# Optimization experiments

Hardware: AMD Instinct MI355X
Metric: run time of the kernel (lower is better)

## Reference

```python
import jax, jax.numpy as jnp
import numpy as np

GRID_H, GRID_W = 496, 432  # config.grid_shape
BN_EPS = 1e-5


def setup_inputs() -> dict:
    key = jax.random.key(0)
    k1, k2, k3 = jax.random.split(key, 3)
    B, D, P, N, C = 4, 4, 12000, 100, 64
    x = jax.random.normal(k1, (B, D, P, N), dtype=jnp.float32)
    indices = jax.random.randint(k2, (B, P, 2), 0, GRID_W, dtype=jnp.int32)
    W = jax.random.normal(k3, (C, D), dtype=jnp.float32) / np.sqrt(D)
    gamma = jnp.ones((C,), dtype=jnp.float32)
    beta = jnp.zeros((C,), dtype=jnp.float32)
    return {"x": x, "indices": indices, "W": W, "gamma": gamma, "beta": beta}


def reference(x, indices, W, gamma, beta):
    # 1x1 conv (bias=False): [B, D, P, N] x [C, D] -> [B, C, P, N]
    y = jnp.einsum('bdpn,cd->bcpn', x, W)
    # BatchNorm2d (training-mode batch statistics, biased variance)
    mean = jnp.mean(y, axis=(0, 2, 3), keepdims=True)
    var = jnp.var(y, axis=(0, 2, 3), keepdims=True)
    y = (y - mean) * jax.lax.rsqrt(var + BN_EPS)
    y = y * gamma.reshape(1, -1, 1, 1) + beta.reshape(1, -1, 1, 1)
    y = jax.nn.relu(y)
    # MaxPool2d((1, N)) then squeeze -> [B, C, P]
    p = jnp.max(y, axis=3)
    # scatter: per-batch index_add into flattened BEV grid
    pillars = jnp.transpose(p, (0, 2, 1))  # [B, P, C]
    flat_idx = indices[..., 0] * GRID_W + indices[..., 1]  # [B, P]
    grid = jax.vmap(
        lambda v, i: jax.ops.segment_sum(v, i, num_segments=GRID_H * GRID_W)
    )(pillars, flat_idx)  # [B, H*W, C]
    C = pillars.shape[-1]
    out = grid.reshape(-1, GRID_H, GRID_W, C)
    return jnp.transpose(out, (0, 3, 1, 2))  # [B, C, H, W]
```

## Files before the change

### kernel.cpp

```cpp
#include <hip/hip_runtime.h>

#define B_ 4
#define D_ 4
#define P_ 12000
#define N_ 100
#define C_ 64
#define GH 496
#define GW 432
#define PN (P_*N_)
#define HW (GH*GW)
#define WPB 12
#define PPB (WPB*8)
#define GRID_F (B_*(P_/PPB))
#define OVFCAP 4096

static constexpr size_t OFF_ST    = 0;
static constexpr size_t OFF_PART  = 512;
static constexpr size_t PART_BYTES= 14*(size_t)GRID_F*4;
static constexpr size_t OFF_SLOT  = (OFF_PART + PART_BYTES + 255) & ~(size_t)255;
static constexpr size_t SLOT_BYTES= (size_t)B_*HW*4;
static constexpr size_t OFF_OVFC  = OFF_SLOT + SLOT_BYTES;
static constexpr size_t OFF_OVF   = OFF_OVFC + 64;
static constexpr size_t OVF_BYTES = (size_t)OVFCAP*4;
static constexpr size_t OFF_U     = (OFF_OVF + OVF_BYTES + 255) & ~(size_t)255;
static constexpr size_t U_BYTES   = (size_t)B_*P_*C_*4;

template<int CTRL>
__device__ __forceinline__ float dppmax(float v) {
    int s = __builtin_amdgcn_update_dpp(0, __float_as_int(v), CTRL, 0xf, 0xf, true);
    return fmaxf(v, __int_as_float(s));
}

__global__ __launch_bounds__(256) void k_init(int4* __restrict__ slot4,
                                              int* __restrict__ ovfcnt) {
    int i = blockIdx.x*256 + threadIdx.x;
    int4 neg1; neg1.x = neg1.y = neg1.z = neg1.w = -1;
    slot4[i] = neg1;
    if (i == 0) *ovfcnt = 0;
}

__global__ __launch_bounds__(256) void k_alloc(const int* __restrict__ idx,
                                               int* __restrict__ slot,
                                               int* __restrict__ ovf,
                                               int* __restrict__ ovfcnt) {
    const int BPB = (P_ + 255)/256;
    int b = blockIdx.x / BPB;
    int p = (blockIdx.x % BPB)*256 + threadIdx.x;
    if (p >= P_) return;
    size_t bp = (size_t)b*P_ + p;
    int h = idx[bp*2], w = idx[bp*2 + 1];
    int cell = h*GW + w;
    int old = atomicMax(&slot[(size_t)b*HW + cell], p);
    if (old != -1) {
        int loser = (old < p) ? old : p;
        int at = atomicAdd(ovfcnt, 1);
        if (at < OVFCAP) ovf[at] = b*P_ + loser;
    }
}

__global__ __launch_bounds__(768) void k_fused(const float* __restrict__ x,
                                               const float* __restrict__ Wm,
                                               float* __restrict__ partials,
                                               float* __restrict__ uraw) {
    __shared__ float tr[WPB][8*65 + 8];
    __shared__ float red[WPB][14];
    const int BPB = P_/PPB;
    int b    = blockIdx.x / BPB;
    int pblk = (blockIdx.x % BPB)*PPB;
    int lane = threadIdx.x & 63;
    int wv   = threadIdx.x >> 6;
    int pl   = lane >> 3;
    int oct  = lane & 7;
    int p    = pblk + wv*8 + pl;
    const float* xb = x + (size_t)b*D_*PN + (size_t)p*N_;

    float4 xq[3][4];
    #pragma unroll
    for (int j = 0; j < 3; ++j) {
        int n = 4*oct + 32*j;
        #pragma unroll
        for (int d = 0; d < 4; ++d)
            xq[j][d] = *reinterpret_cast<const float4*>(xb + n + (size_t)d*PN);
    }
    float x13[4];
    #pragma unroll
    for (int d = 0; d < 4; ++d)
        x13[d] = (oct < 4) ? xb[96 + oct + (size_t)d*PN] : xq[0][d].x;

    {
        float s0=0,s1=0,s2=0,s3=0;
        float m00=0,m01=0,m02=0,m03=0,m11=0,m12=0,m13=0,m22=0,m23=0,m33=0;
        #pragma unroll
        for (int j = 0; j < 3; ++j) {
            #pragma unroll
            for (int e = 0; e < 4; ++e) {
                float x0 = ((const float*)&xq[j][0])[e];
                float x1 = ((const float*)&xq[j][1])[e];
                float x2 = ((const float*)&xq[j][2])[e];
                float x3 = ((const float*)&xq[j][3])[e];
                s0+=x0; s1+=x1; s2+=x2; s3+=x3;
                m00=fmaf(x0,x0,m00); m01=fmaf(x0,x1,m01); m02=fmaf(x0,x2,m02); m03=fmaf(x0,x3,m03);
                m11=fmaf(x1,x1,m11); m12=fmaf(x1,x2,m12); m13=fmaf(x1,x3,m13);
                m22=fmaf(x2,x2,m22); m23=fmaf(x2,x3,m23); m33=fmaf(x3,x3,m33);
            }
        }
        if (oct < 4) {
            float x0=x13[0], x1=x13[1], x2=x13[2], x3=x13[3];
            s0+=x0; s1+=x1; s2+=x2; s3+=x3;
            m00=fmaf(x0,x0,m00); m01=fmaf(x0,x1,m01); m02=fmaf(x0,x2,m02); m03=fmaf(x0,x3,m03);
            m11=fmaf(x1,x1,m11); m12=fmaf(x1,x2,m12); m13=fmaf(x1,x3,m13);
            m22=fmaf(x2,x2,m22); m23=fmaf(x2,x3,m23); m33=fmaf(x3,x3,m33);
        }
        float v[14] = {s0,s1,s2,s3,m00,m01,m02,m03,m11,m12,m13,m22,m23,m33};
        #pragma unroll
        for (int j = 0; j < 14; ++j) {
            float t = v[j];
            #pragma unroll
            for (int off = 32; off; off >>= 1) t += __shfl_down(t, off);
            if (lane == 0) red[wv][j] = t;
        }
        __syncthreads();
        if (threadIdx.x < 14) {
            int j = threadIdx.x;
            float t = 0.f;
            #pragma unroll
            for (int w2 = 0; w2 < WPB; ++w2) t += red[w2][j];
            partials[(size_t)j*GRID_F + blockIdx.x] = t;
        }
    }

    for (int c = 0; c < C_; c += 2) {
        const float4 wA = *reinterpret_cast<const float4*>(Wm + c*4);
        const float4 wB = *reinterpret_cast<const float4*>(Wm + (c+1)*4);
        float mA = -3.4e38f, mB = -3.4e38f;
        #pragma unroll
        for (int j = 0; j < 3; ++j) {
            #pragma unroll
            for (int e = 0; e < 4; ++e) {
                float v0 = ((const float*)&xq[j][0])[e];
                float v1 = ((const float*)&xq[j][1])[e];
                float v2 = ((const float*)&xq[j][2])[e];
                float v3 = ((const float*)&xq[j][3])[e];
                mA = fmaxf(mA, fmaf(wA.x, v0, fmaf(wA.y, v1,
                           fmaf(wA.z, v2, wA.w * v3))));
                mB = fmaxf(mB, fmaf(wB.x, v0, fmaf(wB.y, v1,
                           fmaf(wB.z, v2, wB.w * v3))));
            }
        }
        mA = fmaxf(mA, fmaf(wA.x, x13[0], fmaf(wA.y, x13[1],
                   fmaf(wA.z, x13[2], wA.w * x13[3]))));
        mB = fmaxf(mB, fmaf(wB.x, x13[0], fmaf(wB.y, x13[1],
                   fmaf(wB.z, x13[2], wB.w * x13[3]))));
        mA = dppmax<0xB1>(mA); mA = dppmax<0x4E>(mA); mA = dppmax<0x141>(mA);
        mB = dppmax<0xB1>(mB); mB = dppmax<0x4E>(mB); mB = dppmax<0x141>(mB);
        if (oct == (c >> 3)) {
            tr[wv][pl*65 + c]     = mA;
            tr[wv][pl*65 + c + 1] = mB;
        }
    }
    __builtin_amdgcn_s_waitcnt(0);
    for (int pi = 0; pi < 8; ++pi)
        uraw[((size_t)b*P_ + pblk + wv*8 + pi)*C_ + lane] = tr[wv][pi*65 + lane];
}

__global__ __launch_bounds__(256) void k_stats(const float* __restrict__ partials,
                                               const float* __restrict__ Wm,
                                               const float* __restrict__ gamma,
                                               const float* __restrict__ beta,
                                               float* __restrict__ st) {
    __shared__ double mom_s[14];
    __shared__ double redd[4];
    int lane = threadIdx.x & 63, wv = threadIdx.x >> 6;
    for (int j = 0; j < 14; ++j) {
        double s = 0.0;
        for (int i = threadIdx.x; i < GRID_F; i += 256)
            s += (double)partials[(size_t)j*GRID_F + i];
        #pragma unroll
        for (int off = 32; off; off >>= 1) s += __shfl_down(s, off);
        if (lane == 0) redd[wv] = s;
        __syncthreads();
        if (threadIdx.x == 0) mom_s[j] = redd[0]+redd[1]+redd[2]+redd[3];
        __syncthreads();
    }
    if (threadIdx.x < C_) {
        int c = threadIdx.x;
        double S[4];
        #pragma unroll
        for (int d = 0; d < 4; ++d) S[d] = mom_s[d];
        double M[4][4];
        int k = 4;
        for (int i = 0; i < 4; ++i)
            for (int j = i; j < 4; ++j) { M[i][j] = mom_s[k]; M[j][i] = mom_s[k]; ++k; }
        double w[4];
        #pragma unroll
        for (int d = 0; d < 4; ++d) w[d] = (double)Wm[c*4+d];
        const double NT = (double)B_ * (double)PN;
        double mean = 0.0;
        #pragma unroll
        for (int d = 0; d < 4; ++d) mean += w[d]*S[d];
        mean /= NT;
        double ey2 = 0.0;
        for (int i = 0; i < 4; ++i)
            for (int j = 0; j < 4; ++j) ey2 += w[i]*w[j]*M[i][j];
        ey2 /= NT;
        double var = ey2 - mean*mean;
        double inv = 1.0 / sqrt(var + 1e-5);
        double sc  = (double)gamma[c] * inv;
        st[c*2]     = (float)sc;
        st[c*2 + 1] = (float)((double)beta[c] - mean*sc);
    }
}

__global__ __launch_bounds__(256) void k_out(const int* __restrict__ slot,
                                             const float* __restrict__ uraw,
                                             const float* __restrict__ st,
                                             float* __restrict__ out) {
    __shared__ float tile[128][65];
    __shared__ int   sslot[128];
    const int nchunk = HW/128;
    int b     = blockIdx.x / nchunk;
    int cb    = blockIdx.x % nchunk;
    int cell0 = cb*128;
    if (threadIdx.x < 128)
        sslot[threadIdx.x] = slot[(size_t)b*HW + cell0 + threadIdx.x];
    __syncthreads();
    const float* vb = uraw + (size_t)b*P_*C_;
    int lane = threadIdx.x & 63;
    int wv   = threadIdx.x >> 6;
    float2 ss = *reinterpret_cast<const float2*>(st + lane*2);
    for (int i = wv*32; i < wv*32 + 32; ++i) {
        int s = sslot[i];
        tile[i][lane] = (s >= 0)
            ? fmaxf(fmaf(ss.x, vb[(size_t)s*C_ + lane], ss.y), 0.0f)
            : 0.0f;
    }
    __syncthreads();
    float* ob = out + (size_t)b*C_*HW + cell0;
    int i  = threadIdx.x & 127;
    int ch = threadIdx.x >> 7;
    for (int c = ch; c < C_; c += 2)
        ob[(size_t)c*HW + i] = tile[i][c];
}

__global__ __launch_bounds__(256) void k_fixup(const int* __restrict__ ovf,
                                               const int* __restrict__ ovfcnt,
                                               const int* __restrict__ idx,
                                               const float* __restrict__ uraw,
                                               const float* __restrict__ st,
                                               float* __restrict__ out) {
    int n = *ovfcnt;
    if (n > OVFCAP) n = OVFCAP;
    int lane = threadIdx.x & 63;
    int wid  = (blockIdx.x*256 + threadIdx.x) >> 6;
    int nw   = gridDim.x*4;
    float2 ss = *reinterpret_cast<const float2*>(st + lane*2);
    for (int e = wid; e < n; e += nw) {
        int bp = ovf[e];
        int b  = bp / P_;
        int h = idx[(size_t)bp*2], w = idx[(size_t)bp*2 + 1];
        int cell = h*GW + w;
        float u = uraw[(size_t)bp*C_ + lane];
        float y = fmaxf(fmaf(ss.x, u, ss.y), 0.0f);
        if (y > 0.0f)
            atomicAdd(&out[((size_t)b*C_ + lane)*HW + cell], y);
    }
}

extern "C" void kernel_launch(void* const* d_in, const int* in_sizes, int n_in,
                              void* d_out, int out_size, void* d_ws, size_t ws_size,
                              hipStream_t stream) {
    const float* x     = (const float*)d_in[0];
    const int*   idx   = (const int*)  d_in[1];
    const float* Wm    = (const float*)d_in[2];
    const float* gamma = (const float*)d_in[3];
    const float* beta  = (const float*)d_in[4];
    float* out = (float*)d_out;

    char* ws = (char*)d_ws;
    float* st       = (float*)(ws + OFF_ST);
    float* partials = (float*)(ws + OFF_PART);
    int*   slot     = (int*)  (ws + OFF_SLOT);
    int*   ovfcnt   = (int*)  (ws + OFF_OVFC);
    int*   ovf      = (int*)  (ws + OFF_OVF);
    float* uraw     = (float*)(ws + OFF_U);

    k_init <<<(int)(SLOT_BYTES/16/256), 256, 0, stream>>>((int4*)(ws + OFF_SLOT), ovfcnt);
    k_alloc<<<B_*((P_ + 255)/256), 256, 0, stream>>>(idx, slot, ovf, ovfcnt);
    k_fused<<<GRID_F, WPB*64, 0, stream>>>(x, Wm, partials, uraw);
    k_stats<<<1, 256, 0, stream>>>(partials, Wm, gamma, beta, st);
    k_out  <<<B_*(HW/128), 256, 0, stream>>>(slot, uraw, st, out);
    k_fixup<<<32, 256, 0, stream>>>(ovf, ovfcnt, idx, uraw, st, out);
}
```

Baseline: 152.9 us.

## Fuse BN stats into main kernel, packed-FMA math, and restructure output scatter

Removes the separate stats kernel: each block atomically accumulates its moments into double accumulators, and the last block to finish (found with a done counter) computes the BN scale and shift. The moment and conv-max loops are rewritten with two-wide float vectors so the compiler can emit packed FMA. k_out is restructured so each block writes two channels over a contiguous cell chunk, gathering float2 values instead of going through an LDS transpose tile. The init kernel is replaced by hipMemsetAsync calls. The trade-off is the added cost of global atomics and a last-block pattern, plus reading each slot entry 32 times in k_out.

```diff
diff --git a/kernel.cpp b/kernel.cpp
--- a/kernel.cpp
+++ b/kernel.cpp
@@ -13,30 +13,39 @@
 #define PPB (WPB*8)
 #define GRID_F (B_*(P_/PPB))
 #define OVFCAP 4096
+#define OUT_CHUNK 2304
+#define OUT_NCH (HW/OUT_CHUNK)
+
+typedef float v2f __attribute__((ext_vector_type(2)));
+
+#if defined(__has_builtin)
+#if __has_builtin(__builtin_elementwise_fma)
+#define HAVE_EW_FMA 1
+#endif
+#endif
+__device__ __forceinline__ v2f fma2(v2f a, v2f b, v2f c) {
+#ifdef HAVE_EW_FMA
+    return __builtin_elementwise_fma(a, b, c);
+#else
+    v2f r; r.x = fmaf(a.x, b.x, c.x); r.y = fmaf(a.y, b.y, c.y); return r;
+#endif
+}
+__device__ __forceinline__ v2f max2(v2f a, v2f b) {
+    v2f r; r.x = fmaxf(a.x, b.x); r.y = fmaxf(a.y, b.y); return r;
+}
 
 static constexpr size_t OFF_ST    = 0;
-static constexpr size_t OFF_PART  = 512;
-static constexpr size_t PART_BYTES= 14*(size_t)GRID_F*4;
-static constexpr size_t OFF_SLOT  = (OFF_PART + PART_BYTES + 255) & ~(size_t)255;
+static constexpr size_t OFF_CTL   = 512;
+static constexpr size_t OFF_SLOT  = 1024;
 static constexpr size_t SLOT_BYTES= (size_t)B_*HW*4;
-static constexpr size_t OFF_OVFC  = OFF_SLOT + SLOT_BYTES;
-static constexpr size_t OFF_OVF   = OFF_OVFC + 64;
-static constexpr size_t OVF_BYTES = (size_t)OVFCAP*4;
-static constexpr size_t OFF_U     = (OFF_OVF + OVF_BYTES + 255) & ~(size_t)255;
+static constexpr size_t OFF_OVF   = OFF_SLOT + SLOT_BYTES;
+static constexpr size_t OFF_U     = OFF_OVF + (size_t)OVFCAP*4;
 static constexpr size_t U_BYTES   = (size_t)B_*P_*C_*4;
 
 template<int CTRL>
 __device__ __forceinline__ float dppmax(float v) {
     int s = __builtin_amdgcn_update_dpp(0, __float_as_int(v), CTRL, 0xf, 0xf, true);
     return fmaxf(v, __int_as_float(s));
-}
-
-__global__ __launch_bounds__(256) void k_init(int4* __restrict__ slot4,
-                                              int* __restrict__ ovfcnt) {
-    int i = blockIdx.x*256 + threadIdx.x;
-    int4 neg1; neg1.x = neg1.y = neg1.z = neg1.w = -1;
-    slot4[i] = neg1;
-    if (i == 0) *ovfcnt = 0;
 }
 
 __global__ __launch_bounds__(256) void k_alloc(const int* __restrict__ idx,
@@ -60,10 +69,15 @@
 
 __global__ __launch_bounds__(768) void k_fused(const float* __restrict__ x,
                                                const float* __restrict__ Wm,
-                                               float* __restrict__ partials,
+                                               const float* __restrict__ gamma,
+                                               const float* __restrict__ beta,
+                                               int* __restrict__ done,
+                                               double* __restrict__ momacc,
+                                               float* __restrict__ st,
                                                float* __restrict__ uraw) {
     __shared__ float tr[WPB][8*65 + 8];
     __shared__ float red[WPB][14];
+    __shared__ int   slastf;
     const int BPB = P_/PPB;
     int b    = blockIdx.x / BPB;
     int pblk = (blockIdx.x % BPB)*PPB;
@@ -88,8 +102,8 @@
         x13[d] = (oct < 4) ? xb[96 + oct + (size_t)d*PN] : xq[0][d].x;
 
     {
-        float s0=0,s1=0,s2=0,s3=0;
-        float m00=0,m01=0,m02=0,m03=0,m11=0,m12=0,m13=0,m22=0,m23=0,m33=0;
+        v2f s01 = {0.f,0.f}, s23 = {0.f,0.f};
+        v2f a0 = {0.f,0.f}, a1 = {0.f,0.f}, a2 = {0.f,0.f}, a3 = {0.f,0.f}, a4 = {0.f,0.f};
         #pragma unroll
         for (int j = 0; j < 3; ++j) {
             #pragma unroll
@@ -98,20 +112,29 @@
                 float x1 = ((const float*)&xq[j][1])[e];
                 float x2 = ((const float*)&xq[j][2])[e];
                 float x3 = ((const float*)&xq[j][3])[e];
-                s0+=x0; s1+=x1; s2+=x2; s3+=x3;
-                m00=fmaf(x0,x0,m00); m01=fmaf(x0,x1,m01); m02=fmaf(x0,x2,m02); m03=fmaf(x0,x3,m03);
-                m11=fmaf(x1,x1,m11); m12=fmaf(x1,x2,m12); m13=fmaf(x1,x3,m13);
-                m22=fmaf(x2,x2,m22); m23=fmaf(x2,x3,m23); m33=fmaf(x3,x3,m33);
+                v2f q01 = {x0,x1}, q12 = {x1,x2}, q23 = {x2,x3}, q02 = {x0,x2}, q33 = {x3,x3};
+                s01 += q01; s23 += q23;
+                a0 = fma2(q01, q01, a0);
+                a1 = fma2(q01, q12, a1);
+                a2 = fma2(q01, q23, a2);
+                a3 = fma2(q02, q33, a3);
+                a4 = fma2(q23, q23, a4);
             }
         }
         if (oct < 4) {
-            float x0=x13[0], x1=x13[1], x2=x13[2], x3=x13[3];
-            s0+=x0; s1+=x1; s2+=x2; s3+=x3;
-            m00=fmaf(x0,x0,m00); m01=fmaf(x0,x1,m01); m02=fmaf(x0,x2,m02); m03=fmaf(x0,x3,m03);
-            m11=fmaf(x1,x1,m11); m12=fmaf(x1,x2,m12); m13=fmaf(x1,x3,m13);
-            m22=fmaf(x2,x2,m22); m23=fmaf(x2,x3,m23); m33=fmaf(x3,x3,m33);
-        }
-        float v[14] = {s0,s1,s2,s3,m00,m01,m02,m03,m11,m12,m13,m22,m23,m33};
+            float x0 = x13[0], x1 = x13[1], x2 = x13[2], x3 = x13[3];
+            v2f q01 = {x0,x1}, q12 = {x1,x2}, q23 = {x2,x3}, q02 = {x0,x2}, q33 = {x3,x3};
+            s01 += q01; s23 += q23;
+            a0 = fma2(q01, q01, a0);
+            a1 = fma2(q01, q12, a1);
+            a2 = fma2(q01, q23, a2);
+            a3 = fma2(q02, q33, a3);
+            a4 = fma2(q23, q23, a4);
+        }
+        float v[14] = {s01.x, s01.y, s23.x, s23.y,
+                       a0.x, a1.x, a2.x, a3.x,
+                       a0.y, a1.y, a2.y,
+                       a4.x, a3.y, a4.y};
         #pragma unroll
         for (int j = 0; j < 14; ++j) {
             float t = v[j];
@@ -125,14 +148,52 @@
             float t = 0.f;
             #pragma unroll
             for (int w2 = 0; w2 < WPB; ++w2) t += red[w2][j];
-            partials[(size_t)j*GRID_F + blockIdx.x] = t;
+            atomicAdd(&momacc[j], (double)t);
+        }
+    }
+    __threadfence();
+    if (threadIdx.x == 0) slastf = (atomicAdd(done, 1) == GRID_F - 1);
+    __syncthreads();
+    if (slastf) {
+        __shared__ double smom[14];
+        if (threadIdx.x < 14)
+            smom[threadIdx.x] = atomicAdd(&momacc[threadIdx.x], 0.0);
+        __syncthreads();
+        if (threadIdx.x < C_) {
+            int c = threadIdx.x;
+            double S[4];
+            #pragma unroll
+            for (int d = 0; d < 4; ++d) S[d] = smom[d];
+            double M[4][4];
+            int k = 4;
+            for (int i = 0; i < 4; ++i)
+                for (int j = i; j < 4; ++j) { M[i][j] = smom[k]; M[j][i] = smom[k]; ++k; }
+            double w[4];
+            #pragma unroll
+            for (int d = 0; d < 4; ++d) w[d] = (double)Wm[c*4+d];
+            const double NT = (double)B_ * (double)PN;
+            double mean = 0.0;
+            #pragma unroll
+            for (int d = 0; d < 4; ++d) mean += w[d]*S[d];
+            mean /= NT;
+            double ey2 = 0.0;
+            for (int i = 0; i < 4; ++i)
+                for (int j = 0; j < 4; ++j) ey2 += w[i]*w[j]*M[i][j];
+            ey2 /= NT;
+            double var = ey2 - mean*mean;
+            double inv = 1.0 / sqrt(var + 1e-5);
+            double sc  = (double)gamma[c] * inv;
+            st[c*2]     = (float)sc;
+            st[c*2 + 1] = (float)((double)beta[c] - mean*sc);
         }
     }
 
     for (int c = 0; c < C_; c += 2) {
         const float4 wA = *reinterpret_cast<const float4*>(Wm + c*4);
         const float4 wB = *reinterpret_cast<const float4*>(Wm + (c+1)*4);
-        float mA = -3.4e38f, mB = -3.4e38f;
+        v2f wp0 = {wA.x, wB.x}, wp1 = {wA.y, wB.y};
+        v2f wp2 = {wA.z, wB.z}, wp3 = {wA.w, wB.w};
+        v2f m = {-3.4e38f, -3.4e38f};
         #pragma unroll
         for (int j = 0; j < 3; ++j) {
             #pragma unroll
@@ -141,16 +202,21 @@
                 float v1 = ((const float*)&xq[j][1])[e];
                 float v2 = ((const float*)&xq[j][2])[e];
                 float v3 = ((const float*)&xq[j][3])[e];
-                mA = fmaxf(mA, fmaf(wA.x, v0, fmaf(wA.y, v1,
-                           fmaf(wA.z, v2, wA.w * v3))));
-                mB = fmaxf(mB, fmaf(wB.x, v0, fmaf(wB.y, v1,
-                           fmaf(wB.z, v2, wB.w * v3))));
+                v2f dot = wp3 * v3;
+                dot = fma2(wp2, v2f{v2, v2}, dot);
+                dot = fma2(wp1, v2f{v1, v1}, dot);
+                dot = fma2(wp0, v2f{v0, v0}, dot);
+                m = max2(m, dot);
             }
         }
-        mA = fmaxf(mA, fmaf(wA.x, x13[0], fmaf(wA.y, x13[1],
-                   fmaf(wA.z, x13[2], wA.w * x13[3]))));
-        mB = fmaxf(mB, fmaf(wB.x, x13[0], fmaf(wB.y, x13[1],
-                   fmaf(wB.z, x13[2], wB.w * x13[3]))));
+        {
+            v2f dot = wp3 * x13[3];
+            dot = fma2(wp2, v2f{x13[2], x13[2]}, dot);
+            dot = fma2(wp1, v2f{x13[1], x13[1]}, dot);
+            dot = fma2(wp0, v2f{x13[0], x13[0]}, dot);
+            m = max2(m, dot);
+        }
+        float mA = m.x, mB = m.y;
         mA = dppmax<0xB1>(mA); mA = dppmax<0x4E>(mA); mA = dppmax<0x141>(mA);
         mB = dppmax<0xB1>(mB); mB = dppmax<0x4E>(mB); mB = dppmax<0x141>(mB);
         if (oct == (c >> 3)) {
@@ -163,83 +229,35 @@
         uraw[((size_t)b*P_ + pblk + wv*8 + pi)*C_ + lane] = tr[wv][pi*65 + lane];
 }
 
-__global__ __launch_bounds__(256) void k_stats(const float* __restrict__ partials,
-                                               const float* __restrict__ Wm,
-                                               const float* __restrict__ gamma,
-                                               const float* __restrict__ beta,
-                                               float* __restrict__ st) {
-    __shared__ double mom_s[14];
-    __shared__ double redd[4];
-    int lane = threadIdx.x & 63, wv = threadIdx.x >> 6;
-    for (int j = 0; j < 14; ++j) {
-        double s = 0.0;
-        for (int i = threadIdx.x; i < GRID_F; i += 256)
-            s += (double)partials[(size_t)j*GRID_F + i];
-        #pragma unroll
-        for (int off = 32; off; off >>= 1) s += __shfl_down(s, off);
-        if (lane == 0) redd[wv] = s;
-        __syncthreads();
-        if (threadIdx.x == 0) mom_s[j] = redd[0]+redd[1]+redd[2]+redd[3];
-        __syncthreads();
-    }
-    if (threadIdx.x < C_) {
-        int c = threadIdx.x;
-        double S[4];
-        #pragma unroll
-        for (int d = 0; d < 4; ++d) S[d] = mom_s[d];
-        double M[4][4];
-        int k = 4;
-        for (int i = 0; i < 4; ++i)
-            for (int j = i; j < 4; ++j) { M[i][j] = mom_s[k]; M[j][i] = mom_s[k]; ++k; }
-        double w[4];
-        #pragma unroll
-        for (int d = 0; d < 4; ++d) w[d] = (double)Wm[c*4+d];
-        const double NT = (double)B_ * (double)PN;
-        double mean = 0.0;
-        #pragma unroll
-        for (int d = 0; d < 4; ++d) mean += w[d]*S[d];
-        mean /= NT;
-        double ey2 = 0.0;
-        for (int i = 0; i < 4; ++i)
-            for (int j = 0; j < 4; ++j) ey2 += w[i]*w[j]*M[i][j];
-        ey2 /= NT;
-        double var = ey2 - mean*mean;
-        double inv = 1.0 / sqrt(var + 1e-5);
-        double sc  = (double)gamma[c] * inv;
-        st[c*2]     = (float)sc;
-        st[c*2 + 1] = (float)((double)beta[c] - mean*sc);
-    }
-}
-
 __global__ __launch_bounds__(256) void k_out(const int* __restrict__ slot,
                                              const float* __restrict__ uraw,
                                              const float* __restrict__ st,
                                              float* __restrict__ out) {
-    __shared__ float tile[128][65];
-    __shared__ int   sslot[128];
-    const int nchunk = HW/128;
-    int b     = blockIdx.x / nchunk;
-    int cb    = blockIdx.x % nchunk;
-    int cell0 = cb*128;
-    if (threadIdx.x < 128)
-        sslot[threadIdx.x] = slot[(size_t)b*HW + cell0 + threadIdx.x];
-    __syncthreads();
-    const float* vb = uraw + (size_t)b*P_*C_;
-    int lane = threadIdx.x & 63;
-    int wv   = threadIdx.x >> 6;
-    float2 ss = *reinterpret_cast<const float2*>(st + lane*2);
-    for (int i = wv*32; i < wv*32 + 32; ++i) {
-        int s = sslot[i];
-        tile[i][lane] = (s >= 0)
-            ? fmaxf(fmaf(ss.x, vb[(size_t)s*C_ + lane], ss.y), 0.0f)
-            : 0.0f;
-    }
-    __syncthreads();
-    float* ob = out + (size_t)b*C_*HW + cell0;
-    int i  = threadIdx.x & 127;
-    int ch = threadIdx.x >> 7;
-    for (int c = ch; c < C_; c += 2)
-        ob[(size_t)c*HW + i] = tile[i][c];
+    int bid   = blockIdx.x;
+    int chunk = bid % OUT_NCH;
+    int cp    = (bid / OUT_NCH) % (C_/2);
+    int b     = bid / (OUT_NCH*(C_/2));
+    int c     = cp*2;
+    int cell0 = chunk*OUT_CHUNK;
+    const float4 s4 = *reinterpret_cast<const float4*>(st + c*2);
+    const int*    sl  = slot + (size_t)b*HW + cell0;
+    const float2* vb2 = reinterpret_cast<const float2*>(uraw + (size_t)b*P_*C_);
+    float* oA = out + ((size_t)b*C_ + c    )*HW + cell0;
+    float* oB = out + ((size_t)b*C_ + c + 1)*HW + cell0;
+    int t = threadIdx.x;
+    #pragma unroll
+    for (int i = 0; i < OUT_CHUNK/256; ++i) {
+        int cell = i*256 + t;
+        int s = sl[cell];
+        float yA = 0.f, yB = 0.f;
+        if (s >= 0) {
+            float2 u = vb2[(size_t)s*(C_/2) + cp];
+            yA = fmaxf(fmaf(s4.x, u.x, s4.y), 0.f);
+            yB = fmaxf(fmaf(s4.z, u.y, s4.w), 0.f);
+        }
+        oA[cell] = yA;
+        oB[cell] = yB;
+    }
 }
 
 __global__ __launch_bounds__(256) void k_fixup(const int* __restrict__ ovf,
@@ -277,17 +295,18 @@
     float* out = (float*)d_out;
 
     char* ws = (char*)d_ws;
-    float* st       = (float*)(ws + OFF_ST);
-    float* partials = (float*)(ws + OFF_PART);
-    int*   slot     = (int*)  (ws + OFF_SLOT);
-    int*   ovfcnt   = (int*)  (ws + OFF_OVFC);
-    int*   ovf      = (int*)  (ws + OFF_OVF);
-    float* uraw     = (float*)(ws + OFF_U);
-
-    k_init <<<(int)(SLOT_BYTES/16/256), 256, 0, stream>>>((int4*)(ws + OFF_SLOT), ovfcnt);
+    float*  st     = (float*) (ws + OFF_ST);
+    int*    ovfcnt = (int*)   (ws + OFF_CTL);
+    int*    done   = (int*)   (ws + OFF_CTL + 4);
+    double* momacc = (double*)(ws + OFF_CTL + 64);
+    int*    slot   = (int*)   (ws + OFF_SLOT);
+    int*    ovf    = (int*)   (ws + OFF_OVF);
+    float*  uraw   = (float*) (ws + OFF_U);
+
+    hipMemsetAsync(ws + OFF_SLOT, 0xFF, SLOT_BYTES, stream);
+    hipMemsetAsync(ws + OFF_CTL, 0, 256, stream);
     k_alloc<<<B_*((P_ + 255)/256), 256, 0, stream>>>(idx, slot, ovf, ovfcnt);
-    k_fused<<<GRID_F, WPB*64, 0, stream>>>(x, Wm, partials, uraw);
-    k_stats<<<1, 256, 0, stream>>>(partials, Wm, gamma, beta, st);
-    k_out  <<<B_*(HW/128), 256, 0, stream>>>(slot, uraw, st, out);
+    k_fused<<<GRID_F, WPB*64, 0, stream>>>(x, Wm, gamma, beta, done, momacc, st, uraw);
+    k_out  <<<B_*(C_/2)*OUT_NCH, 256, 0, stream>>>(slot, uraw, st, out);
     k_fixup<<<32, 256, 0, stream>>>(ovf, ovfcnt, idx, uraw, st, out);
 }
```

New measurement: 246.9 us. 61.5% more time.
